# Kernel tuning notes

Hardware: AMD Instinct MI355X
Metric: run time of the kernel (lower is better)

Reference implementation:

```python
import jax, jax.numpy as jnp
import numpy as np


def setup_inputs() -> dict:
    key = jax.random.key(0)
    k1, k2 = jax.random.split(key)
    B, C, H, W = 8, 64, 64, 64
    x = jax.random.normal(k1, (B, C, H, W), dtype=jnp.float32)
    stdv = 1.0 / np.sqrt(C)
    weight = jax.random.uniform(k2, (C, C), dtype=jnp.float32, minval=-stdv, maxval=stdv)
    return {"x": x, "weight": weight}


def reference(x, weight):
    B, C, H, W = x.shape
    N = H * W
    xf = x.reshape(B, C, N)            # [B, C, N]
    g_x = jnp.transpose(xf, (0, 2, 1))  # [B, N, C] (also theta_x)
    # f[b, i, j] = sum_c x[b, c, i] * x[b, c, j]
    f = jnp.einsum('bic,bcj->bij', g_x, xf)  # [B, N, N]
    adj = jax.nn.softmax(f, axis=-1)
    support = jnp.einsum('bnc,cd->bnd', g_x, weight)  # [B, N, C]
    y = jnp.einsum('bij,bjc->bic', adj, support)      # [B, N, C]
    y = jnp.transpose(y, (0, 2, 1)).reshape(B, C, H, W)
    return y + x
```

## Files before the change

### kernel.cpp

```cpp
#include <hip/hip_runtime.h>
#include <stdint.h>


#define NTOK 4096
#define CCH  64
#define LOG2E 1.44269504088896340736f

typedef float v4f __attribute__((ext_vector_type(4)));
typedef __bf16 v8bf __attribute__((ext_vector_type(8)));
typedef unsigned short v8us __attribute__((ext_vector_type(8)));

__device__ __forceinline__ unsigned short f2bf(float f) {
    union { float f; unsigned int u; } c; c.f = f;
    unsigned int r = c.u + 0x7fffu + ((c.u >> 16) & 1u);
    return (unsigned short)(r >> 16);
}

__device__ __forceinline__ v8bf ld8(const unsigned short* p) {
    union { v8us s; v8bf b; } u;
    u.s = *(const v8us*)p;
    return u.b;
}

__device__ __forceinline__ unsigned int pkbf(float a, float b) {
    union { float f; unsigned int u; } ua, ub; ua.f = a; ub.f = b;
    return __builtin_amdgcn_perm(ub.u, ua.u, 0x07060302u);
}

__device__ __forceinline__ void gload_lds16(const void* g, void* l) {
    __builtin_amdgcn_global_load_lds(
        (const __attribute__((address_space(1))) unsigned int*)g,
        (__attribute__((address_space(3))) unsigned int*)l,
        16, 0, 0);
}

__global__ __launch_bounds__(256) void prep_kernel(
    const float* __restrict__ x,
    const float* __restrict__ w,
    unsigned short* __restrict__ xT,
    unsigned short* __restrict__ sT)
{
    __shared__ float Xf[64 * 65];

    const int tid  = threadIdx.x;
    const int lane = tid & 63;
    const int wv   = __builtin_amdgcn_readfirstlane(tid >> 6);
    const int b    = blockIdx.y;
    const int n0   = blockIdx.x * 64;

    const float* xb = x + (size_t)b * CCH * NTOK + n0 + lane;
    #pragma unroll
    for (int k = 0; k < 16; ++k) {
        const int c = wv * 16 + k;
        Xf[c * 65 + lane] = xb[(size_t)c * NTOK];
    }
    __syncthreads();

    {
        const int n  = tid >> 2;
        const int c0 = (tid & 3) * 16;
        unsigned int pk[8];
        #pragma unroll
        for (int k = 0; k < 8; ++k) {
            const float a = Xf[(c0 + 2 * k) * 65 + n];
            const float c2 = Xf[(c0 + 2 * k + 1) * 65 + n];
            pk[k] = (unsigned int)f2bf(a) | ((unsigned int)f2bf(c2) << 16);
        }
        unsigned short* xtr = xT + ((size_t)b * NTOK + n0 + n) * CCH + c0;
        *(uint4*)(xtr)     = *(uint4*)(pk);
        *(uint4*)(xtr + 8) = *(uint4*)(pk + 4);
    }

    float acc[16];
    #pragma unroll
    for (int d = 0; d < 16; ++d) acc[d] = 0.f;

    #pragma unroll 4
    for (int c = 0; c < 64; ++c) {
        const float xc = Xf[c * 65 + lane];
        const float* wr = w + c * 64 + wv * 16;
        #pragma unroll
        for (int d = 0; d < 16; ++d) acc[d] = fmaf(xc, wr[d], acc[d]);
    }
    unsigned short* stb = sT + (size_t)b * CCH * NTOK + n0 + lane;
    #pragma unroll
    for (int d = 0; d < 16; ++d)
        stb[(size_t)(wv * 16 + d) * NTOK] = f2bf(acc[d]);
}

__global__ __launch_bounds__(256, 2) void flash_kernel(
    const unsigned short* __restrict__ xT,
    const unsigned short* __restrict__ sT,
    float* __restrict__ part_o,
    float* __restrict__ part_l,
    int nchunk, int chunk_len)
{
    __shared__ __align__(16) unsigned short Kt[64 * 64];
    __shared__ __align__(16) unsigned short Vt[64 * 64];
    __shared__ __align__(16) unsigned short Pt[4][64 * 64];

    const int tid  = threadIdx.x;
    const int w    = tid >> 6;
    const int lane = tid & 63;
    const int quad = lane >> 4;
    const int l16  = lane & 15;
    const int l7   = l16 & 7;
    const int b     = blockIdx.z;
    const int chunk = blockIdx.y;
    const int i0   = blockIdx.x * 256;
    const int irow = i0 + w * 64;
    const int jb   = chunk * chunk_len;

    const unsigned short* xTb = xT + (size_t)b * NTOK * CCH;
    const unsigned short* sTb = sT + (size_t)b * CCH * NTOK;

    const int srow = w * 8 + (lane >> 3);
    const int sc   = (lane & 7) ^ (lane >> 3);
    unsigned short* kd0 = Kt + w * 512;
    unsigned short* vd0 = Vt + w * 512;

    v8bf aq0[4], aq1[4];
    #pragma unroll
    for (int m = 0; m < 4; ++m) {
        const unsigned short* qr = xTb + (size_t)(irow + m * 16 + l16) * CCH + quad * 8;
        aq0[m] = ld8(qr);
        aq1[m] = ld8(qr + 32);
    }

    float negml2[4];
    #pragma unroll
    for (int m = 0; m < 4; ++m) {
        float msq = 0.f;
        #pragma unroll
        for (int i = 0; i < 8; ++i) {
            float e0 = (float)aq0[m][i], e1 = (float)aq1[m][i];
            msq = fmaf(e0, e0, msq);
            msq = fmaf(e1, e1, msq);
        }
        msq += __shfl_xor(msq, 16);
        msq += __shfl_xor(msq, 32);
        negml2[m] = -msq * LOG2E;
    }

    v8bf ones;
    #pragma unroll
    for (int i = 0; i < 8; ++i) ones[i] = (__bf16)1.0f;

    v4f o[4][4];
    v4f lsum[4];
    #pragma unroll
    for (int m = 0; m < 4; ++m) {
        lsum[m][0]=0.f; lsum[m][1]=0.f; lsum[m][2]=0.f; lsum[m][3]=0.f;
        #pragma unroll
        for (int ct = 0; ct < 4; ++ct) { o[m][ct][0]=0.f; o[m][ct][1]=0.f; o[m][ct][2]=0.f; o[m][ct][3]=0.f; }
    }

    unsigned short* Pw = Pt[w];
    const int phalf = (quad & 1) * 4;
    const int pgq   = quad >> 1;

    for (int jj = 0; jj < chunk_len; jj += 64) {
        const int j0 = jb + jj;

        gload_lds16(xTb + (size_t)(j0 + srow) * CCH + sc * 8,       kd0);
        gload_lds16(xTb + (size_t)(j0 + 32 + srow) * CCH + sc * 8,  kd0 + 2048);
        gload_lds16(sTb + (size_t)srow * NTOK + j0 + sc * 8,        vd0);
        gload_lds16(sTb + (size_t)(32 + srow) * NTOK + j0 + sc * 8, vd0 + 2048);
        __syncthreads();

        #pragma unroll
        for (int jt = 0; jt < 4; ++jt) {
            const int krow = 16 * jt + l16;
            const unsigned short* kb = Kt + krow * 64;
            const int c0 = quad ^ (krow & 7);
            v8bf bk0 = ld8(kb + c0 * 8);
            v8bf bk1 = ld8(kb + (c0 ^ 4) * 8);
            #pragma unroll
            for (int m = 0; m < 4; ++m) {
                v4f z; z[0]=0.f; z[1]=0.f; z[2]=0.f; z[3]=0.f;
                z = __builtin_amdgcn_mfma_f32_16x16x32_bf16(bk0, aq0[m], z, 0, 0, 0);
                z = __builtin_amdgcn_mfma_f32_16x16x32_bf16(bk1, aq1[m], z, 0, 0, 0);
                const float p0 = exp2f(fmaf(z[0], LOG2E, negml2[m]));
                const float p1 = exp2f(fmaf(z[1], LOG2E, negml2[m]));
                const float p2 = exp2f(fmaf(z[2], LOG2E, negml2[m]));
                const float p3 = exp2f(fmaf(z[3], LOG2E, negml2[m]));
                uint2 pk; pk.x = pkbf(p0, p1); pk.y = pkbf(p2, p3);
                const int pos = (2 * jt + pgq) ^ l7;
                *(uint2*)(Pw + (m * 16 + l16) * 64 + pos * 8 + phalf) = pk;
            }
        }

        v8bf pb0[4], pb1[4];
        #pragma unroll
        for (int m = 0; m < 4; ++m) {
            const unsigned short* pr = Pw + (m * 16 + l16) * 64;
            const int p0c = quad ^ l7;
            pb0[m] = ld8(pr + p0c * 8);
            pb1[m] = ld8(pr + (p0c ^ 4) * 8);
            lsum[m] = __builtin_amdgcn_mfma_f32_16x16x32_bf16(ones, pb0[m], lsum[m], 0, 0, 0);
            lsum[m] = __builtin_amdgcn_mfma_f32_16x16x32_bf16(ones, pb1[m], lsum[m], 0, 0, 0);
        }

        #pragma unroll
        for (int ct = 0; ct < 4; ++ct) {
            const int vrow = 16 * ct + l16;
            const unsigned short* vb = Vt + vrow * 64;
            const int c0 = quad ^ (vrow & 7);
            v8bf bv0 = ld8(vb + c0 * 8);
            v8bf bv1 = ld8(vb + (c0 ^ 4) * 8);
            #pragma unroll
            for (int m = 0; m < 4; ++m) {
                o[m][ct] = __builtin_amdgcn_mfma_f32_16x16x32_bf16(bv0, pb0[m], o[m][ct], 0, 0, 0);
                o[m][ct] = __builtin_amdgcn_mfma_f32_16x16x32_bf16(bv1, pb1[m], o[m][ct], 0, 0, 0);
            }
        }
        __syncthreads();
    }

    const size_t pbase = (size_t)(b * nchunk + chunk) * NTOK + irow;
    #pragma unroll
    for (int m = 0; m < 4; ++m)
        if (quad == 0) part_l[pbase + m * 16 + l16] = lsum[m][0];
    float* po = part_o + pbase * 64;
    #pragma unroll
    for (int m = 0; m < 4; ++m)
        #pragma unroll
        for (int ct = 0; ct < 4; ++ct)
            *(v4f*)(po + (size_t)(m * 16 + l16) * 64 + ct * 16 + quad * 4) = o[m][ct];
}

template <int KS_>
__global__ __launch_bounds__(256, 2) void combine_kernel(
    const float* __restrict__ part_o,
    const float* __restrict__ part_l,
    const float* __restrict__ x,
    float* __restrict__ out)
{
    __shared__ float Of[64 * 65];
    const int tid = threadIdx.x;
    const int b = blockIdx.y;
    const int i0 = blockIdx.x * 64;
    const int row = tid >> 2;
    const int seg = tid & 3;

    float acc[16];
    #pragma unroll
    for (int k = 0; k < 16; ++k) acc[k] = 0.f;
    float lt = 0.f;

    #pragma unroll
    for (int ch = 0; ch < KS_; ++ch) {
        const size_t base = (size_t)(b * KS_ + ch) * NTOK + i0 + row;
        lt += part_l[base];
        const float* po = part_o + base * 64 + seg * 16;
        #pragma unroll
        for (int k = 0; k < 4; ++k) {
            float4 v = *(const float4*)(po + k * 4);
            acc[k*4+0] += v.x; acc[k*4+1] += v.y; acc[k*4+2] += v.z; acc[k*4+3] += v.w;
        }
    }
    const float inv = 1.f / lt;
    #pragma unroll
    for (int k = 0; k < 16; ++k) Of[row * 65 + seg * 16 + k] = acc[k] * inv;
    __syncthreads();

    const int c    = tid >> 2;
    const int part = tid & 3;
    const float* xrow = x   + ((size_t)b * CCH + c) * NTOK + i0 + part * 16;
    float*       orow = out + ((size_t)b * CCH + c) * NTOK + i0 + part * 16;
    #pragma unroll
    for (int i4 = 0; i4 < 4; ++i4) {
        float4 xv = *(const float4*)(xrow + i4 * 4);
        float4 ov;
        ov.x = Of[(part * 16 + i4 * 4 + 0) * 65 + c] + xv.x;
        ov.y = Of[(part * 16 + i4 * 4 + 1) * 65 + c] + xv.y;
        ov.z = Of[(part * 16 + i4 * 4 + 2) * 65 + c] + xv.z;
        ov.w = Of[(part * 16 + i4 * 4 + 3) * 65 + c] + xv.w;
        *(float4*)(orow + i4 * 4) = ov;
    }
}

extern "C" void kernel_launch(void* const* d_in, const int* in_sizes, int n_in,
                              void* d_out, int out_size, void* d_ws, size_t ws_size,
                              hipStream_t stream) {
    const float* x = (const float*)d_in[0];
    const float* w = (const float*)d_in[1];
    float* out = (float*)d_out;

    const size_t xT_elems = (size_t)8 * NTOK * CCH;
    unsigned short* xT = (unsigned short*)d_ws;
    unsigned short* sT = xT + xT_elems;
    char* rest = (char*)d_ws + 2 * xT_elems * sizeof(unsigned short);

    int KS = 4;
    while (KS > 1) {
        size_t need = 2 * xT_elems * sizeof(unsigned short)
                    + (size_t)KS * ((size_t)8 * NTOK * CCH * 4 + (size_t)8 * NTOK * 4);
        if (need <= ws_size) break;
        KS >>= 1;
    }
    float* part_o = (float*)rest;
    float* part_l = (float*)(rest + (size_t)KS * 8 * NTOK * CCH * 4);

    dim3 gp(64, 8);
    prep_kernel<<<gp, 256, 0, stream>>>(x, w, xT, sT);
    dim3 gf(16, KS, 8);
    flash_kernel<<<gf, 256, 0, stream>>>(xT, sT, part_o, part_l, KS, NTOK / KS);
    dim3 gc(64, 8);
    if (KS == 4)      combine_kernel<4><<<gc, 256, 0, stream>>>(part_o, part_l, x, out);
    else if (KS == 2) combine_kernel<2><<<gc, 256, 0, stream>>>(part_o, part_l, x, out);
    else              combine_kernel<1><<<gc, 256, 0, stream>>>(part_o, part_l, x, out);
}
```

Measured before the change: 139.2 us.

## Shrink flash query tile, raise split-K to 8, and use MFMA for support projection

The flash kernel now gives each wave 32 query rows instead of 64, halving per-block rows and the P scratch buffer, and raises the occupancy hint to 4 blocks. Key/value splits go from 4 to 8 when workspace allows, so the grid grows from 512 to 2048 blocks to fill the GPU. The combine kernel is retiled to 32 rows per block and templated for 8 splits. The prep kernel's scalar-FMA x·W projection is replaced with bf16 MFMA over a swizzled LDS copy. This trades more partial-output traffic and K/V reloads, and lower-precision weights, for better parallelism.

```diff
diff --git a/kernel.cpp b/kernel.cpp
--- a/kernel.cpp
+++ b/kernel.cpp
@@ -41,10 +41,13 @@
     unsigned short* __restrict__ sT)
 {
     __shared__ float Xf[64 * 65];
+    __shared__ __align__(16) unsigned short Xb[64 * 64];
 
     const int tid  = threadIdx.x;
     const int lane = tid & 63;
     const int wv   = __builtin_amdgcn_readfirstlane(tid >> 6);
+    const int quad = lane >> 4;
+    const int l16  = lane & 15;
     const int b    = blockIdx.y;
     const int n0   = blockIdx.x * 64;
 
@@ -62,33 +65,47 @@
         unsigned int pk[8];
         #pragma unroll
         for (int k = 0; k < 8; ++k) {
-            const float a = Xf[(c0 + 2 * k) * 65 + n];
+            const float a  = Xf[(c0 + 2 * k) * 65 + n];
             const float c2 = Xf[(c0 + 2 * k + 1) * 65 + n];
             pk[k] = (unsigned int)f2bf(a) | ((unsigned int)f2bf(c2) << 16);
         }
         unsigned short* xtr = xT + ((size_t)b * NTOK + n0 + n) * CCH + c0;
         *(uint4*)(xtr)     = *(uint4*)(pk);
         *(uint4*)(xtr + 8) = *(uint4*)(pk + 4);
-    }
-
-    float acc[16];
-    #pragma unroll
-    for (int d = 0; d < 16; ++d) acc[d] = 0.f;
-
-    #pragma unroll 4
-    for (int c = 0; c < 64; ++c) {
-        const float xc = Xf[c * 65 + lane];
-        const float* wr = w + c * 64 + wv * 16;
-        #pragma unroll
-        for (int d = 0; d < 16; ++d) acc[d] = fmaf(xc, wr[d], acc[d]);
-    }
-    unsigned short* stb = sT + (size_t)b * CCH * NTOK + n0 + lane;
-    #pragma unroll
-    for (int d = 0; d < 16; ++d)
-        stb[(size_t)(wv * 16 + d) * NTOK] = f2bf(acc[d]);
-}
-
-__global__ __launch_bounds__(256, 2) void flash_kernel(
+        const int g0 = c0 >> 3;
+        *(uint4*)(Xb + (n << 6) + ((g0 ^ (n & 7)) << 3))       = *(uint4*)(pk);
+        *(uint4*)(Xb + (n << 6) + (((g0 + 1) ^ (n & 7)) << 3)) = *(uint4*)(pk + 4);
+    }
+    __syncthreads();
+
+    v8bf aw0[4], aw1[4];
+    #pragma unroll
+    for (int dt = 0; dt < 4; ++dt) {
+        #pragma unroll
+        for (int j = 0; j < 8; ++j) {
+            aw0[dt][j] = (__bf16)w[(quad * 8 + j) * 64 + dt * 16 + l16];
+            aw1[dt][j] = (__bf16)w[(quad * 8 + j + 32) * 64 + dt * 16 + l16];
+        }
+    }
+    const int nrow = wv * 16 + l16;
+    const unsigned short* xr = Xb + (nrow << 6);
+    const int cc = quad ^ (nrow & 7);
+    const v8bf bx0 = ld8(xr + (cc << 3));
+    const v8bf bx1 = ld8(xr + ((cc ^ 4) << 3));
+
+    unsigned short* stb = sT + (size_t)b * CCH * NTOK + n0 + wv * 16 + l16;
+    #pragma unroll
+    for (int dt = 0; dt < 4; ++dt) {
+        v4f z; z[0]=0.f; z[1]=0.f; z[2]=0.f; z[3]=0.f;
+        z = __builtin_amdgcn_mfma_f32_16x16x32_bf16(aw0[dt], bx0, z, 0, 0, 0);
+        z = __builtin_amdgcn_mfma_f32_16x16x32_bf16(aw1[dt], bx1, z, 0, 0, 0);
+        #pragma unroll
+        for (int r = 0; r < 4; ++r)
+            stb[(size_t)(dt * 16 + quad * 4 + r) * NTOK] = f2bf(z[r]);
+    }
+}
+
+__global__ __launch_bounds__(256, 4) void flash_kernel(
     const unsigned short* __restrict__ xT,
     const unsigned short* __restrict__ sT,
     float* __restrict__ part_o,
@@ -97,7 +114,7 @@
 {
     __shared__ __align__(16) unsigned short Kt[64 * 64];
     __shared__ __align__(16) unsigned short Vt[64 * 64];
-    __shared__ __align__(16) unsigned short Pt[4][64 * 64];
+    __shared__ __align__(16) unsigned short Pt[4][32 * 64];
 
     const int tid  = threadIdx.x;
     const int w    = tid >> 6;
@@ -107,8 +124,8 @@
     const int l7   = l16 & 7;
     const int b     = blockIdx.z;
     const int chunk = blockIdx.y;
-    const int i0   = blockIdx.x * 256;
-    const int irow = i0 + w * 64;
+    const int i0   = blockIdx.x * 128;
+    const int irow = i0 + w * 32;
     const int jb   = chunk * chunk_len;
 
     const unsigned short* xTb = xT + (size_t)b * NTOK * CCH;
@@ -119,17 +136,17 @@
     unsigned short* kd0 = Kt + w * 512;
     unsigned short* vd0 = Vt + w * 512;
 
-    v8bf aq0[4], aq1[4];
-    #pragma unroll
-    for (int m = 0; m < 4; ++m) {
+    v8bf aq0[2], aq1[2];
+    #pragma unroll
+    for (int m = 0; m < 2; ++m) {
         const unsigned short* qr = xTb + (size_t)(irow + m * 16 + l16) * CCH + quad * 8;
         aq0[m] = ld8(qr);
         aq1[m] = ld8(qr + 32);
     }
 
-    float negml2[4];
-    #pragma unroll
-    for (int m = 0; m < 4; ++m) {
+    float negml2[2];
+    #pragma unroll
+    for (int m = 0; m < 2; ++m) {
         float msq = 0.f;
         #pragma unroll
         for (int i = 0; i < 8; ++i) {
@@ -146,10 +163,10 @@
     #pragma unroll
     for (int i = 0; i < 8; ++i) ones[i] = (__bf16)1.0f;
 
-    v4f o[4][4];
-    v4f lsum[4];
-    #pragma unroll
-    for (int m = 0; m < 4; ++m) {
+    v4f o[2][4];
+    v4f lsum[2];
+    #pragma unroll
+    for (int m = 0; m < 2; ++m) {
         lsum[m][0]=0.f; lsum[m][1]=0.f; lsum[m][2]=0.f; lsum[m][3]=0.f;
         #pragma unroll
         for (int ct = 0; ct < 4; ++ct) { o[m][ct][0]=0.f; o[m][ct][1]=0.f; o[m][ct][2]=0.f; o[m][ct][3]=0.f; }
@@ -176,7 +193,7 @@
             v8bf bk0 = ld8(kb + c0 * 8);
             v8bf bk1 = ld8(kb + (c0 ^ 4) * 8);
             #pragma unroll
-            for (int m = 0; m < 4; ++m) {
+            for (int m = 0; m < 2; ++m) {
                 v4f z; z[0]=0.f; z[1]=0.f; z[2]=0.f; z[3]=0.f;
                 z = __builtin_amdgcn_mfma_f32_16x16x32_bf16(bk0, aq0[m], z, 0, 0, 0);
                 z = __builtin_amdgcn_mfma_f32_16x16x32_bf16(bk1, aq1[m], z, 0, 0, 0);
@@ -190,9 +207,9 @@
             }
         }
 
-        v8bf pb0[4], pb1[4];
-        #pragma unroll
-        for (int m = 0; m < 4; ++m) {
+        v8bf pb0[2], pb1[2];
+        #pragma unroll
+        for (int m = 0; m < 2; ++m) {
             const unsigned short* pr = Pw + (m * 16 + l16) * 64;
             const int p0c = quad ^ l7;
             pb0[m] = ld8(pr + p0c * 8);
@@ -209,7 +226,7 @@
             v8bf bv0 = ld8(vb + c0 * 8);
             v8bf bv1 = ld8(vb + (c0 ^ 4) * 8);
             #pragma unroll
-            for (int m = 0; m < 4; ++m) {
+            for (int m = 0; m < 2; ++m) {
                 o[m][ct] = __builtin_amdgcn_mfma_f32_16x16x32_bf16(bv0, pb0[m], o[m][ct], 0, 0, 0);
                 o[m][ct] = __builtin_amdgcn_mfma_f32_16x16x32_bf16(bv1, pb1[m], o[m][ct], 0, 0, 0);
             }
@@ -219,63 +236,62 @@
 
     const size_t pbase = (size_t)(b * nchunk + chunk) * NTOK + irow;
     #pragma unroll
-    for (int m = 0; m < 4; ++m)
+    for (int m = 0; m < 2; ++m)
         if (quad == 0) part_l[pbase + m * 16 + l16] = lsum[m][0];
     float* po = part_o + pbase * 64;
     #pragma unroll
-    for (int m = 0; m < 4; ++m)
+    for (int m = 0; m < 2; ++m)
         #pragma unroll
         for (int ct = 0; ct < 4; ++ct)
             *(v4f*)(po + (size_t)(m * 16 + l16) * 64 + ct * 16 + quad * 4) = o[m][ct];
 }
 
 template <int KS_>
-__global__ __launch_bounds__(256, 2) void combine_kernel(
+__global__ __launch_bounds__(256) void combine_kernel(
     const float* __restrict__ part_o,
     const float* __restrict__ part_l,
     const float* __restrict__ x,
     float* __restrict__ out)
 {
-    __shared__ float Of[64 * 65];
+    __shared__ float Of[32 * 65];
     const int tid = threadIdx.x;
     const int b = blockIdx.y;
-    const int i0 = blockIdx.x * 64;
-    const int row = tid >> 2;
-    const int seg = tid & 3;
-
-    float acc[16];
-    #pragma unroll
-    for (int k = 0; k < 16; ++k) acc[k] = 0.f;
+    const int i0 = blockIdx.x * 32;
+
+    const int row = tid >> 3;
+    const int col = (tid & 7) * 8;
+    float acc[8];
+    #pragma unroll
+    for (int k = 0; k < 8; ++k) acc[k] = 0.f;
     float lt = 0.f;
 
     #pragma unroll
     for (int ch = 0; ch < KS_; ++ch) {
         const size_t base = (size_t)(b * KS_ + ch) * NTOK + i0 + row;
         lt += part_l[base];
-        const float* po = part_o + base * 64 + seg * 16;
-        #pragma unroll
-        for (int k = 0; k < 4; ++k) {
-            float4 v = *(const float4*)(po + k * 4);
-            acc[k*4+0] += v.x; acc[k*4+1] += v.y; acc[k*4+2] += v.z; acc[k*4+3] += v.w;
-        }
+        const float* po = part_o + base * 64 + col;
+        float4 v0 = *(const float4*)(po);
+        float4 v1 = *(const float4*)(po + 4);
+        acc[0]+=v0.x; acc[1]+=v0.y; acc[2]+=v0.z; acc[3]+=v0.w;
+        acc[4]+=v1.x; acc[5]+=v1.y; acc[6]+=v1.z; acc[7]+=v1.w;
     }
     const float inv = 1.f / lt;
     #pragma unroll
-    for (int k = 0; k < 16; ++k) Of[row * 65 + seg * 16 + k] = acc[k] * inv;
+    for (int k = 0; k < 8; ++k) Of[row * 65 + col + k] = acc[k] * inv;
     __syncthreads();
 
     const int c    = tid >> 2;
     const int part = tid & 3;
-    const float* xrow = x   + ((size_t)b * CCH + c) * NTOK + i0 + part * 16;
-    float*       orow = out + ((size_t)b * CCH + c) * NTOK + i0 + part * 16;
-    #pragma unroll
-    for (int i4 = 0; i4 < 4; ++i4) {
+    const float* xrow = x   + ((size_t)b * CCH + c) * NTOK + i0 + part * 8;
+    float*       orow = out + ((size_t)b * CCH + c) * NTOK + i0 + part * 8;
+    #pragma unroll
+    for (int i4 = 0; i4 < 2; ++i4) {
         float4 xv = *(const float4*)(xrow + i4 * 4);
         float4 ov;
-        ov.x = Of[(part * 16 + i4 * 4 + 0) * 65 + c] + xv.x;
-        ov.y = Of[(part * 16 + i4 * 4 + 1) * 65 + c] + xv.y;
-        ov.z = Of[(part * 16 + i4 * 4 + 2) * 65 + c] + xv.z;
-        ov.w = Of[(part * 16 + i4 * 4 + 3) * 65 + c] + xv.w;
+        ov.x = Of[(part * 8 + i4 * 4 + 0) * 65 + c] + xv.x;
+        ov.y = Of[(part * 8 + i4 * 4 + 1) * 65 + c] + xv.y;
+        ov.z = Of[(part * 8 + i4 * 4 + 2) * 65 + c] + xv.z;
+        ov.w = Of[(part * 8 + i4 * 4 + 3) * 65 + c] + xv.w;
         *(float4*)(orow + i4 * 4) = ov;
     }
 }
@@ -292,7 +308,7 @@
     unsigned short* sT = xT + xT_elems;
     char* rest = (char*)d_ws + 2 * xT_elems * sizeof(unsigned short);
 
-    int KS = 4;
+    int KS = 8;
     while (KS > 1) {
         size_t need = 2 * xT_elems * sizeof(unsigned short)
                     + (size_t)KS * ((size_t)8 * NTOK * CCH * 4 + (size_t)8 * NTOK * 4);
@@ -304,10 +320,11 @@
 
     dim3 gp(64, 8);
     prep_kernel<<<gp, 256, 0, stream>>>(x, w, xT, sT);
-    dim3 gf(16, KS, 8);
+    dim3 gf(32, KS, 8);
     flash_kernel<<<gf, 256, 0, stream>>>(xT, sT, part_o, part_l, KS, NTOK / KS);
-    dim3 gc(64, 8);
-    if (KS == 4)      combine_kernel<4><<<gc, 256, 0, stream>>>(part_o, part_l, x, out);
+    dim3 gc(128, 8);
+    if (KS == 8)      combine_kernel<8><<<gc, 256, 0, stream>>>(part_o, part_l, x, out);
+    else if (KS == 4) combine_kernel<4><<<gc, 256, 0, stream>>>(part_o, part_l, x, out);
     else if (KS == 2) combine_kernel<2><<<gc, 256, 0, stream>>>(part_o, part_l, x, out);
     else              combine_kernel<1><<<gc, 256, 0, stream>>>(part_o, part_l, x, out);
 }
```

Measured after the change: 133.3 us. -4.3%, faster.
